# Performance work log

Measured on AMD Instinct MI355X. Metric: run time of the kernel, lower is better.

## Reference

```python
import jax, jax.numpy as jnp
import numpy as np

B, S, I, H = 1024, 1024, 32, 128

def setup_inputs() -> dict:
    key = jax.random.key(0)
    ks = jax.random.split(key, 10)
    def xavier(k, shape):
        fan_in, fan_out = shape
        bound = float(np.sqrt(6.0 / (fan_in + fan_out)))
        return jax.random.uniform(k, shape, jnp.float32, -bound, bound)
    return {
        "x": jax.random.normal(ks[0], (B, S, I), jnp.float32),
        "W_r": xavier(ks[1], (I, H)), "U_r": xavier(ks[2], (H, H)), "b_r": jnp.zeros((H,), jnp.float32),
        "W_z": xavier(ks[3], (I, H)), "U_z": xavier(ks[4], (H, H)), "b_z": jnp.zeros((H,), jnp.float32),
        "W_h": xavier(ks[5], (I, H)), "U_h": xavier(ks[6], (H, H)), "b_h": jnp.zeros((H,), jnp.float32),
    }

def reference(x, W_r, U_r, b_r, W_z, U_z, b_z, W_h, U_h, b_h):
    # x: [B, S, I]. Precompute all input projections in one big GEMM each (math-identical,
    # since x_t @ W is independent across t), then scan the sequential recurrence.
    xz = jnp.einsum('bsi,ih->bsh', x, W_z) + b_z  # [B,S,H]
    xh = jnp.einsum('bsi,ih->bsh', x, W_h) + b_h  # [B,S,H]
    # r_t = sigmoid(x@W_r + h@U_r + b_r) is computed in the original but never used
    # (h_tilde is NOT gated by r), so it has no effect on the output.

    h0 = jnp.zeros((x.shape[0], U_z.shape[0]), x.dtype)  # [B,H]

    def step(h, inp):
        xz_t, xh_t = inp  # each [B,H]
        z = jax.nn.sigmoid(xz_t + h @ U_z)
        hh = jnp.tanh(xh_t + h @ U_h)
        h_new = (1.0 - z) * h + z * hh  # note: swapped vs standard GRU, faithful to source
        return h_new, h_new

    # scan over time: [S,B,H]
    xs = (jnp.swapaxes(xz, 0, 1), jnp.swapaxes(xh, 0, 1))
    h_last, hs = jax.lax.scan(step, h0, xs)
    hidden_seq = jnp.swapaxes(hs, 0, 1)  # [B,S,H]
    return hidden_seq, h_last[None]  # final state keeps leading dim of 1, as in source
```

## Files before the change

kernel.cpp:

```cpp
#include <hip/hip_runtime.h>
#include <hip/hip_bf16.h>

typedef __bf16 bf16x8 __attribute__((ext_vector_type(8)));
typedef float  f32x4  __attribute__((ext_vector_type(4)));
typedef unsigned short u16;
typedef unsigned int   u32;
typedef unsigned int   u32x2 __attribute__((ext_vector_type(2)));
typedef unsigned long long u64;

#define NB 1024
#define NS 1024
#define NI 32
#define NH 128
#define NCH (NS / 8)

__device__ __forceinline__ u64 pack4_bf16(f32x4 v) {
  u32 lo, hi;
  asm("v_cvt_pk_bf16_f32 %0, %1, %2" : "=v"(lo) : "v"(v[0]), "v"(v[1]));
  asm("v_cvt_pk_bf16_f32 %0, %1, %2" : "=v"(hi) : "v"(v[2]), "v"(v[3]));
  u32x2 p; p[0] = lo; p[1] = hi;
  return __builtin_bit_cast(u64, p);
}

__device__ __forceinline__ void lds_barrier() {
  __builtin_amdgcn_sched_barrier(0);
  asm volatile("s_waitcnt lgkmcnt(0)" ::: "memory");
  __builtin_amdgcn_s_barrier();
  asm volatile("" ::: "memory");
  __builtin_amdgcn_sched_barrier(0);
}

__global__ __launch_bounds__(512, 2) void gru_scan(
    const float* __restrict__ x,
    const float* __restrict__ Wz, const float* __restrict__ Uz, const float* __restrict__ bz,
    const float* __restrict__ Wh, const float* __restrict__ Uh, const float* __restrict__ bh,
    float* __restrict__ out)
{
  __shared__ __align__(16) u64    hbuf[2][16][32];
  __shared__ __align__(16) bf16x8 xbuf[2][8][16][4];

  const int tid  = threadIdx.x;
  const int lane = tid & 63;
  const int w    = tid >> 6;
  const int ml   = lane & 15;
  const int g    = lane >> 4;
  const int rb   = blockIdx.x * 16;

  bf16x8 ufrag[2][4];
  bf16x8 wfrag[2];
  f32x4  bias2[2];
  {
    const float* Ug[2] = {Uz, Uh};
    const float* Wg[2] = {Wz, Wh};
    const float* bg[2] = {bz, bh};
    const int n0 = 16 * w + ml;
#pragma unroll
    for (int gate = 0; gate < 2; ++gate) {
#pragma unroll
      for (int kt = 0; kt < 4; ++kt)
#pragma unroll
        for (int j = 0; j < 8; ++j)
          ufrag[gate][kt][j] = (__bf16)Ug[gate][(32 * kt + 8 * g + j) * NH + n0];
#pragma unroll
      for (int j = 0; j < 8; ++j)
        wfrag[gate][j] = (__bf16)Wg[gate][(8 * g + j) * NH + n0];
      const int nb = 16 * w + 4 * g;
#pragma unroll
      for (int r = 0; r < 4; ++r) bias2[gate][r] = bg[gate][nb + r];
    }
  }

  for (int i = tid; i < 16 * 32; i += 512) hbuf[0][i >> 5][i & 31] = 0ULL;

  const int r_st  = tid >> 5;
  const int c8    = tid & 31;
  const int tt_st = c8 >> 2;
  const int un_st = (c8 & 3) ^ (r_st & 3);
  const float* xbase = x + (size_t)(rb + r_st) * (NS * NI) + c8 * 8;

  {
    f32x4 a0 = *(const f32x4*)(xbase);
    f32x4 a1 = *(const f32x4*)(xbase + 4);
    bf16x8 u;
#pragma unroll
    for (int j = 0; j < 4; ++j) { u[j] = (__bf16)a0[j]; u[4 + j] = (__bf16)a1[j]; }
    xbuf[0][tt_st][r_st][un_st] = u;
  }
  __syncthreads();

  const int sw = (ml & 7) << 1;
  int ridx[4];
#pragma unroll
  for (int kt = 0; kt < 4; ++kt) ridx[kt] = (8 * kt + 2 * g) ^ sw;
  const int widx = (4 * w + g) ^ sw;
  const int xidx = g ^ (ml & 3);

  f32x4 hv = {0.f, 0.f, 0.f, 0.f};
  float* optr = out + (size_t)(rb + ml) * NS * NH + 16 * w + 4 * g;

  f32x4 vxa, vxb;
  const float NL2E  = -1.4426950408889634f;
  const float P2L2E =  2.8853900817779268f;
  const f32x4 zero4 = {0.f, 0.f, 0.f, 0.f};

  f32x4 axz, axh;
  {
    bf16x8 xf = xbuf[0][0][ml][xidx];
    axz = __builtin_amdgcn_mfma_f32_16x16x32_bf16(wfrag[0], xf, bias2[0], 0, 0, 0);
    axh = __builtin_amdgcn_mfma_f32_16x16x32_bf16(wfrag[1], xf, bias2[1], 0, 0, 0);
  }

#define GRU_STEP(P, XB, TT, DO_STORE, DO_STAGE)                                            \
  {                                                                                        \
                                                                     \
    const u64* hrow = &hbuf[P][ml][0];                                                     \
    bf16x8 hf0 = *(const bf16x8*)(hrow + ridx[0]);                                         \
    bf16x8 hf1 = *(const bf16x8*)(hrow + ridx[1]);                                         \
    bf16x8 hf2 = *(const bf16x8*)(hrow + ridx[2]);                                         \
    bf16x8 hf3 = *(const bf16x8*)(hrow + ridx[3]);                                         \
                                         \
    f32x4 z1 = __builtin_amdgcn_mfma_f32_16x16x32_bf16(ufrag[0][0], hf0, axz,   0, 0, 0);  \
    f32x4 h1 = __builtin_amdgcn_mfma_f32_16x16x32_bf16(ufrag[1][0], hf0, axh,   0, 0, 0);  \
    f32x4 z2 = __builtin_amdgcn_mfma_f32_16x16x32_bf16(ufrag[0][2], hf2, zero4, 0, 0, 0);  \
    f32x4 h2 = __builtin_amdgcn_mfma_f32_16x16x32_bf16(ufrag[1][2], hf2, zero4, 0, 0, 0);  \
    z1 = __builtin_amdgcn_mfma_f32_16x16x32_bf16(ufrag[0][1], hf1, z1, 0, 0, 0);           \
    h1 = __builtin_amdgcn_mfma_f32_16x16x32_bf16(ufrag[1][1], hf1, h1, 0, 0, 0);           \
    z2 = __builtin_amdgcn_mfma_f32_16x16x32_bf16(ufrag[0][3], hf3, z2, 0, 0, 0);           \
    h2 = __builtin_amdgcn_mfma_f32_16x16x32_bf16(ufrag[1][3], hf3, h2, 0, 0, 0);           \
    const f32x4 az = z1 + z2;                                                              \
    const f32x4 ah = h1 + h2;                                                              \
                   \
    f32x4 hn;                                                                              \
    _Pragma("unroll")                                                                      \
    for (int r = 0; r < 4; ++r) {                                                          \
      float ez = __builtin_amdgcn_exp2f(az[r] * NL2E);                                     \
      float zz = __builtin_amdgcn_rcpf(1.f + ez);                                          \
      float eh = __builtin_amdgcn_exp2f(ah[r] * P2L2E);                                    \
      float th = 1.f - 2.f * __builtin_amdgcn_rcpf(1.f + eh);                              \
      hn[r] = __builtin_fmaf(zz, th - hv[r], hv[r]);                                       \
    }                                                                                      \
    hv = hn;                                                                               \
                         \
    hbuf[P ^ 1][ml][widx] = pack4_bf16(hn);                                                \
    if (DO_STAGE) {                  \
      bf16x8 u;                                                                            \
      _Pragma("unroll")                                                                    \
      for (int j = 0; j < 4; ++j) { u[j] = (__bf16)vxa[j]; u[4 + j] = (__bf16)vxb[j]; }    \
      xbuf[(XB) ^ 1][tt_st][r_st][un_st] = u;                                              \
    }                                                                                      \
                                     \
    {                                                                                      \
      bf16x8 xf = xbuf[((TT) == 7) ? ((XB) ^ 1) : (XB)][((TT) + 1) & 7][ml][xidx];         \
      axz = __builtin_amdgcn_mfma_f32_16x16x32_bf16(wfrag[0], xf, bias2[0], 0, 0, 0);      \
      axh = __builtin_amdgcn_mfma_f32_16x16x32_bf16(wfrag[1], xf, bias2[1], 0, 0, 0);      \
    }                                                                                      \
                      \
    if (DO_STORE) { __builtin_nontemporal_store(hn, (f32x4*)optr); optr += NH; }           \
    lds_barrier();                                                                         \
  }

#define CHUNK_BODY(XB, CHUNK, MORE)                                                        \
  {                                                                                        \
    if (MORE) {                                                                            \
      const float* p = xbase + (size_t)((CHUNK) + 1) * (8 * NI);                           \
      vxa = *(const f32x4*)(p); vxb = *(const f32x4*)(p + 4);                              \
    }                                                                                      \
    GRU_STEP(0, XB, 0, true, false)                                                        \
    GRU_STEP(1, XB, 1, true, false)                                                        \
    GRU_STEP(0, XB, 2, true, false)                                                        \
    GRU_STEP(1, XB, 3, true, false)                                                        \
    GRU_STEP(0, XB, 4, true, false)                                                        \
    GRU_STEP(1, XB, 5, true, false)                                                        \
    GRU_STEP(0, XB, 6, true, (MORE))                                                       \
    GRU_STEP(1, XB, 7, true, false)                                                        \
  }

  for (int cp = 0; cp < NCH / 2; ++cp) {
    const int  c0 = 2 * cp;
    const bool m1 = (c0 + 2 < NCH);
    CHUNK_BODY(0, c0,     true)
    CHUNK_BODY(1, c0 + 1, m1)
  }

  const size_t lbase = (size_t)NB * NS * NH + (size_t)(rb + ml) * NH + 16 * w + 4 * g;
  *(f32x4*)(out + lbase) = hv;
}

extern "C" void kernel_launch(void* const* d_in, const int* in_sizes, int n_in,
                              void* d_out, int out_size, void* d_ws, size_t ws_size,
                              hipStream_t stream) {
  const float* x  = (const float*)d_in[0];
  const float* Wz = (const float*)d_in[4];
  const float* Uz = (const float*)d_in[5];
  const float* bz = (const float*)d_in[6];
  const float* Wh = (const float*)d_in[7];
  const float* Uh = (const float*)d_in[8];
  const float* bh = (const float*)d_in[9];
  float* out = (float*)d_out;

  gru_scan<<<dim3(NB / 16), dim3(512), 0, stream>>>(x, Wz, Uz, bz, Wh, Uh, bh, out);
}
```

Before: 469.0 us.

## Fold gate scales into weights, merge sigmoid/tanh update, reorder x-projection MFMAs

Pre-scales U, W and bias by -log2(e) and 2*log2(e) so the exponent inputs come straight from the MFMA accumulators. It rewrites the sigmoid, tanh and blend as a single rational expression that needs one reciprocal per element instead of two, with a clamp on the tanh exponent to avoid overflow. The recurrent MFMAs become two serial chains instead of four split partial sums, and the next step's x-projection MFMAs are issued right after them, before the transcendental math. Staging of x uses packed bf16 convert instructions. Scaling before the bf16 cast slightly changes rounding, and the longer dependent MFMA chains may add latency on the serial recurrence path.

```diff
diff --git a/kernel.cpp b/kernel.cpp
--- a/kernel.cpp
+++ b/kernel.cpp
@@ -6,6 +6,7 @@
 typedef unsigned short u16;
 typedef unsigned int   u32;
 typedef unsigned int   u32x2 __attribute__((ext_vector_type(2)));
+typedef unsigned int   u32x4 __attribute__((ext_vector_type(4)));
 typedef unsigned long long u64;
 
 #define NB 1024
@@ -20,6 +21,15 @@
   asm("v_cvt_pk_bf16_f32 %0, %1, %2" : "=v"(hi) : "v"(v[2]), "v"(v[3]));
   u32x2 p; p[0] = lo; p[1] = hi;
   return __builtin_bit_cast(u64, p);
+}
+
+__device__ __forceinline__ bf16x8 cvt8pk(f32x4 a, f32x4 b) {
+  u32x4 p;
+  asm("v_cvt_pk_bf16_f32 %0, %1, %2" : "=v"(p[0]) : "v"(a[0]), "v"(a[1]));
+  asm("v_cvt_pk_bf16_f32 %0, %1, %2" : "=v"(p[1]) : "v"(a[2]), "v"(a[3]));
+  asm("v_cvt_pk_bf16_f32 %0, %1, %2" : "=v"(p[2]) : "v"(b[0]), "v"(b[1]));
+  asm("v_cvt_pk_bf16_f32 %0, %1, %2" : "=v"(p[3]) : "v"(b[2]), "v"(b[3]));
+  return __builtin_bit_cast(bf16x8, p);
 }
 
 __device__ __forceinline__ void lds_barrier() {
@@ -53,6 +63,7 @@
     const float* Ug[2] = {Uz, Uh};
     const float* Wg[2] = {Wz, Wh};
     const float* bg[2] = {bz, bh};
+    const float  gs[2] = {-1.4426950408889634f, 2.8853900817779268f};
     const int n0 = 16 * w + ml;
 #pragma unroll
     for (int gate = 0; gate < 2; ++gate) {
@@ -60,13 +71,13 @@
       for (int kt = 0; kt < 4; ++kt)
 #pragma unroll
         for (int j = 0; j < 8; ++j)
-          ufrag[gate][kt][j] = (__bf16)Ug[gate][(32 * kt + 8 * g + j) * NH + n0];
+          ufrag[gate][kt][j] = (__bf16)(Ug[gate][(32 * kt + 8 * g + j) * NH + n0] * gs[gate]);
 #pragma unroll
       for (int j = 0; j < 8; ++j)
-        wfrag[gate][j] = (__bf16)Wg[gate][(8 * g + j) * NH + n0];
+        wfrag[gate][j] = (__bf16)(Wg[gate][(8 * g + j) * NH + n0] * gs[gate]);
       const int nb = 16 * w + 4 * g;
 #pragma unroll
-      for (int r = 0; r < 4; ++r) bias2[gate][r] = bg[gate][nb + r];
+      for (int r = 0; r < 4; ++r) bias2[gate][r] = bg[gate][nb + r] * gs[gate];
     }
   }
 
@@ -81,10 +92,7 @@
   {
     f32x4 a0 = *(const f32x4*)(xbase);
     f32x4 a1 = *(const f32x4*)(xbase + 4);
-    bf16x8 u;
-#pragma unroll
-    for (int j = 0; j < 4; ++j) { u[j] = (__bf16)a0[j]; u[4 + j] = (__bf16)a1[j]; }
-    xbuf[0][tt_st][r_st][un_st] = u;
+    xbuf[0][tt_st][r_st][un_st] = cvt8pk(a0, a1);
   }
   __syncthreads();
 
@@ -99,9 +107,8 @@
   float* optr = out + (size_t)(rb + ml) * NS * NH + 16 * w + 4 * g;
 
   f32x4 vxa, vxb;
-  const float NL2E  = -1.4426950408889634f;
-  const float P2L2E =  2.8853900817779268f;
-  const f32x4 zero4 = {0.f, 0.f, 0.f, 0.f};
+  const f32x4 one4   = {1.f, 1.f, 1.f, 1.f};
+  const f32x4 clamp4 = {43.35f, 43.35f, 43.35f, 43.35f};
 
   f32x4 axz, axh;
   {
@@ -112,47 +119,45 @@
 
 #define GRU_STEP(P, XB, TT, DO_STORE, DO_STAGE)                                            \
   {                                                                                        \
-                                                                     \
+                              \
     const u64* hrow = &hbuf[P][ml][0];                                                     \
     bf16x8 hf0 = *(const bf16x8*)(hrow + ridx[0]);                                         \
     bf16x8 hf1 = *(const bf16x8*)(hrow + ridx[1]);                                         \
     bf16x8 hf2 = *(const bf16x8*)(hrow + ridx[2]);                                         \
     bf16x8 hf3 = *(const bf16x8*)(hrow + ridx[3]);                                         \
-                                         \
-    f32x4 z1 = __builtin_amdgcn_mfma_f32_16x16x32_bf16(ufrag[0][0], hf0, axz,   0, 0, 0);  \
-    f32x4 h1 = __builtin_amdgcn_mfma_f32_16x16x32_bf16(ufrag[1][0], hf0, axh,   0, 0, 0);  \
-    f32x4 z2 = __builtin_amdgcn_mfma_f32_16x16x32_bf16(ufrag[0][2], hf2, zero4, 0, 0, 0);  \
-    f32x4 h2 = __builtin_amdgcn_mfma_f32_16x16x32_bf16(ufrag[1][2], hf2, zero4, 0, 0, 0);  \
-    z1 = __builtin_amdgcn_mfma_f32_16x16x32_bf16(ufrag[0][1], hf1, z1, 0, 0, 0);           \
-    h1 = __builtin_amdgcn_mfma_f32_16x16x32_bf16(ufrag[1][1], hf1, h1, 0, 0, 0);           \
-    z2 = __builtin_amdgcn_mfma_f32_16x16x32_bf16(ufrag[0][3], hf3, z2, 0, 0, 0);           \
-    h2 = __builtin_amdgcn_mfma_f32_16x16x32_bf16(ufrag[1][3], hf3, h2, 0, 0, 0);           \
-    const f32x4 az = z1 + z2;                                                              \
-    const f32x4 ah = h1 + h2;                                                              \
-                   \
-    f32x4 hn;                                                                              \
+    bf16x8 xf  = xbuf[((TT) == 7) ? ((XB) ^ 1) : (XB)][((TT) + 1) & 7][ml][xidx];          \
+              \
+    f32x4 cz = __builtin_amdgcn_mfma_f32_16x16x32_bf16(ufrag[0][0], hf0, axz, 0, 0, 0);    \
+    f32x4 ch = __builtin_amdgcn_mfma_f32_16x16x32_bf16(ufrag[1][0], hf0, axh, 0, 0, 0);    \
+    cz = __builtin_amdgcn_mfma_f32_16x16x32_bf16(ufrag[0][1], hf1, cz, 0, 0, 0);           \
+    ch = __builtin_amdgcn_mfma_f32_16x16x32_bf16(ufrag[1][1], hf1, ch, 0, 0, 0);           \
+    cz = __builtin_amdgcn_mfma_f32_16x16x32_bf16(ufrag[0][2], hf2, cz, 0, 0, 0);           \
+    ch = __builtin_amdgcn_mfma_f32_16x16x32_bf16(ufrag[1][2], hf2, ch, 0, 0, 0);           \
+    cz = __builtin_amdgcn_mfma_f32_16x16x32_bf16(ufrag[0][3], hf3, cz, 0, 0, 0);           \
+    ch = __builtin_amdgcn_mfma_f32_16x16x32_bf16(ufrag[1][3], hf3, ch, 0, 0, 0);           \
+                                     \
+    axz = __builtin_amdgcn_mfma_f32_16x16x32_bf16(wfrag[0], xf, bias2[0], 0, 0, 0);        \
+    axh = __builtin_amdgcn_mfma_f32_16x16x32_bf16(wfrag[1], xf, bias2[1], 0, 0, 0);        \
+                              \
+    f32x4 bcl = __builtin_elementwise_min(ch, clamp4);                                     \
+    f32x4 e, f;                                                                            \
     _Pragma("unroll")                                                                      \
     for (int r = 0; r < 4; ++r) {                                                          \
-      float ez = __builtin_amdgcn_exp2f(az[r] * NL2E);                                     \
-      float zz = __builtin_amdgcn_rcpf(1.f + ez);                                          \
-      float eh = __builtin_amdgcn_exp2f(ah[r] * P2L2E);                                    \
-      float th = 1.f - 2.f * __builtin_amdgcn_rcpf(1.f + eh);                              \
-      hn[r] = __builtin_fmaf(zz, th - hv[r], hv[r]);                                       \
+      e[r] = __builtin_amdgcn_exp2f(cz[r]);                                                \
+      f[r] = __builtin_amdgcn_exp2f(bcl[r]);                                               \
     }                                                                                      \
+    f32x4 fp  = f + one4;                                                                  \
+    f32x4 num = (f - one4) - hv * fp;                                                      \
+    f32x4 den = (e + one4) * fp;                                                           \
+    f32x4 rr;                                                                              \
+    _Pragma("unroll")                                                                      \
+    for (int r = 0; r < 4; ++r) rr[r] = __builtin_amdgcn_rcpf(den[r]);                     \
+    f32x4 hn = num * rr + hv;                                                              \
     hv = hn;                                                                               \
                          \
     hbuf[P ^ 1][ml][widx] = pack4_bf16(hn);                                                \
     if (DO_STAGE) {                  \
-      bf16x8 u;                                                                            \
-      _Pragma("unroll")                                                                    \
-      for (int j = 0; j < 4; ++j) { u[j] = (__bf16)vxa[j]; u[4 + j] = (__bf16)vxb[j]; }    \
-      xbuf[(XB) ^ 1][tt_st][r_st][un_st] = u;                                              \
-    }                                                                                      \
-                                     \
-    {                                                                                      \
-      bf16x8 xf = xbuf[((TT) == 7) ? ((XB) ^ 1) : (XB)][((TT) + 1) & 7][ml][xidx];         \
-      axz = __builtin_amdgcn_mfma_f32_16x16x32_bf16(wfrag[0], xf, bias2[0], 0, 0, 0);      \
-      axh = __builtin_amdgcn_mfma_f32_16x16x32_bf16(wfrag[1], xf, bias2[1], 0, 0, 0);      \
+      xbuf[(XB) ^ 1][tt_st][r_st][un_st] = cvt8pk(vxa, vxb);                               \
     }                                                                                      \
                       \
     if (DO_STORE) { __builtin_nontemporal_store(hn, (f32x4*)optr); optr += NH; }           \
```

Result: faster. 424.9 us (-9.4%).
